# Kernel tuning notes

Measured on AMD Instinct MI355X. Metric: run time of the kernel, lower is better.

The kernel has to match this reference:

```python
import jax, jax.numpy as jnp
import numpy as np

N_ATOMS = 100_000
N_PAIRS = 3_200_000


def setup_inputs() -> dict:
    key = jax.random.key(0)
    k0, k1, k2, k3, k4 = jax.random.split(key, 5)
    atomic_numbers = jax.random.randint(k0, (N_ATOMS,), 1, 95, dtype=jnp.int32)
    distances = jax.random.uniform(k1, (N_PAIRS,), jnp.float32, 0.5, 5.0)
    cutoffs = jax.random.uniform(k2, (N_PAIRS,), jnp.float32)
    idx_i = jnp.sort(jax.random.randint(k3, (N_PAIRS,), 0, N_ATOMS, dtype=jnp.int32))
    idx_j = jax.random.randint(k4, (N_PAIRS,), 0, N_ATOMS, dtype=jnp.int32)
    # ZBL parameters (trainable=True defaults from __init__)
    a_coefficient = jnp.array([0.8854], dtype=jnp.float32)
    a_exponent = jnp.array([0.23], dtype=jnp.float32)
    phi_coefficients = jnp.array([0.18175, 0.50986, 0.28022, 0.02817], dtype=jnp.float32)
    phi_exponents = jnp.array([3.1998, 0.94229, 0.4029, 0.20162], dtype=jnp.float32)
    # unit conversion buffers: identity units -> factors = 1.0
    ke = jnp.array([1.0 / (4.0 * np.pi * 0.005526349406)], dtype=jnp.float32)
    distances_model2Ang = jnp.array([1.0], dtype=jnp.float32)
    energies_Hatree2model = jnp.array([1.0], dtype=jnp.float32)
    return dict(atomic_numbers=atomic_numbers, distances=distances, cutoffs=cutoffs,
                idx_i=idx_i, idx_j=idx_j, a_coefficient=a_coefficient,
                a_exponent=a_exponent, phi_coefficients=phi_coefficients,
                phi_exponents=phi_exponents, ke=ke,
                distances_model2Ang=distances_model2Ang,
                energies_Hatree2model=energies_Hatree2model)


def reference(atomic_numbers, distances, cutoffs, idx_i, idx_j,
              a_coefficient, a_exponent, phi_coefficients, phi_exponents,
              ke, distances_model2Ang, energies_Hatree2model):
    Z = atomic_numbers.astype(distances.dtype)            # [N]
    distances_ang = distances * distances_model2Ang        # [P]
    za = Z ** jnp.abs(a_exponent)                          # [N] (a_exponent is [1])
    a_ij = jnp.abs(a_coefficient) / (za[idx_i] + za[idx_j])  # [P]
    arguments = distances / a_ij                           # [P] (faithful: uses model-unit distances)
    # L1-normalized |phi_coefficients|
    abs_c = jnp.abs(phi_coefficients)
    coefficients = abs_c / jnp.sum(abs_c)                  # [4]
    exponents = jnp.abs(phi_exponents)                     # [4]
    # phi[p] = sum_k c_k * exp(-e_k * arg_p)  -> [P,4] intermediate
    phi = jnp.sum(coefficients[None, :] * jnp.exp(-exponents[None, :] * arguments[:, None]), axis=1)
    repulsion = ke * Z[idx_i] * Z[idx_j] / distances_ang * phi * cutoffs  # [P]
    Erep = energies_Hatree2model * jax.ops.segment_sum(repulsion, idx_i, num_segments=N_ATOMS)
    return Erep
```

## Files before the change

kernel.cpp:

```cpp
#include <hip/hip_runtime.h>
#include <hip/hip_bf16.h>
#include <math.h>

#define LOG2E 1.4426950408889634f

__global__ void __launch_bounds__(256)
zbl_prep(const int* __restrict__ Z, unsigned char* __restrict__ z8,
         float* __restrict__ out, int n_atoms, int out_n) {
    int i = blockIdx.x * blockDim.x + threadIdx.x;
    if (i < n_atoms) z8[i] = (unsigned char)Z[i];
    if (i < out_n)   out[i] = 0.0f;
}

template <typename ZT>
__global__ void __launch_bounds__(256)
zbl_pairs(const float* __restrict__ dist, const float* __restrict__ cut,
          const int* __restrict__ idx_i, const int* __restrict__ idx_j,
          const ZT* __restrict__ zt,
          const float* __restrict__ a_coef, const float* __restrict__ a_exp,
          const float* __restrict__ phi_c, const float* __restrict__ phi_e,
          const float* __restrict__ ke, const float* __restrict__ d2a,
          const float* __restrict__ e2m,
          float* __restrict__ out, int n) {
    __shared__ float za_tab[128];

    float aexp   = fabsf(a_exp[0]);
    float inv_ac = __fdividef(1.0f, fabsf(a_coef[0]));
    float c0 = fabsf(phi_c[0]), c1 = fabsf(phi_c[1]),
          c2 = fabsf(phi_c[2]), c3 = fabsf(phi_c[3]);
    float cnorm = __fdividef(1.0f, c0 + c1 + c2 + c3);
    c0 *= cnorm; c1 *= cnorm; c2 *= cnorm; c3 *= cnorm;
    float e0 = fabsf(phi_e[0]) * LOG2E, e1 = fabsf(phi_e[1]) * LOG2E,
          e2 = fabsf(phi_e[2]) * LOG2E, e3 = fabsf(phi_e[3]) * LOG2E;
    float scale = ke[0] * e2m[0];
    float inv_d2a = __fdividef(1.0f, d2a[0]);

    int t = threadIdx.x;
    if (t < 128) za_tab[t] = powf((float)t, aexp);
    __syncthreads();

    int p = blockIdx.x * blockDim.x + t;

    int   ii  = -1;
    float val = 0.0f;
    if (p < n) {
        ii = idx_i[p];
        int jj = idx_j[p];
        int zi = (int)zt[ii];
        int zj = (int)zt[jj];
        float zif = (float)zi, zjf = (float)zj;
        float d   = dist[p];
        float arg = d * (za_tab[zi] + za_tab[zj]) * inv_ac;
        float phi = c0 * exp2f(-e0 * arg) + c1 * exp2f(-e1 * arg)
                  + c2 * exp2f(-e2 * arg) + c3 * exp2f(-e3 * arg);
        float invd = __fdividef(1.0f, d);
        val = scale * zif * zjf * phi * cut[p] * invd * inv_d2a;
    }

    int lane = t & 63;
    #pragma unroll
    for (int off = 1; off < 64; off <<= 1) {
        float ov = __shfl_up(val, (unsigned)off, 64);
        int   oi = __shfl_up(ii, (unsigned)off, 64);
        if (lane >= off && oi == ii) val += ov;
    }
    int nxt = __shfl_down(ii, 1u, 64);
    bool tail = (lane == 63) || (nxt != ii);
    if (p < n && tail) atomicAdd(out + ii, val);
}

extern "C" void kernel_launch(void* const* d_in, const int* in_sizes, int n_in,
                              void* d_out, int out_size, void* d_ws, size_t ws_size,
                              hipStream_t stream) {
    const int*   atomic_numbers = (const int*)  d_in[0];
    const float* distances      = (const float*)d_in[1];
    const float* cutoffs        = (const float*)d_in[2];
    const int*   idx_i          = (const int*)  d_in[3];
    const int*   idx_j          = (const int*)  d_in[4];
    const float* a_coefficient  = (const float*)d_in[5];
    const float* a_exponent     = (const float*)d_in[6];
    const float* phi_coeffs     = (const float*)d_in[7];
    const float* phi_exps       = (const float*)d_in[8];
    const float* ke             = (const float*)d_in[9];
    const float* d2a            = (const float*)d_in[10];
    const float* e2m            = (const float*)d_in[11];
    float* out = (float*)d_out;

    const int n_atoms = in_sizes[0];
    const int n_pairs = in_sizes[1];

    const int block = 256;
    const int grid_pairs = (n_pairs + block - 1) / block;
    const int grid_prep  = (((n_atoms > out_size) ? n_atoms : out_size) + block - 1) / block;

    if (ws_size >= (size_t)n_atoms) {
        unsigned char* z8 = (unsigned char*)d_ws;
        zbl_prep<<<grid_prep, block, 0, stream>>>(
            atomic_numbers, z8, out, n_atoms, out_size);
        zbl_pairs<unsigned char><<<grid_pairs, block, 0, stream>>>(
            distances, cutoffs, idx_i, idx_j, z8,
            a_coefficient, a_exponent, phi_coeffs, phi_exps, ke, d2a, e2m,
            out, n_pairs);
    } else {
        hipMemsetAsync(d_out, 0, (size_t)out_size * sizeof(float), stream);
        zbl_pairs<int><<<grid_pairs, block, 0, stream>>>(
            distances, cutoffs, idx_i, idx_j, atomic_numbers,
            a_coefficient, a_exponent, phi_coeffs, phi_exps, ke, d2a, e2m,
            out, n_pairs);
    }
}
```

Baseline: 127.4 us.

## Process two pairs per thread with vectorized loads and a segmented scan

New measurement: 122.3 us. 1.04x faster.

```diff
diff --git a/kernel.cpp b/kernel.cpp
--- a/kernel.cpp
+++ b/kernel.cpp
@@ -12,16 +12,15 @@
     if (i < out_n)   out[i] = 0.0f;
 }
 
-template <typename ZT>
 __global__ void __launch_bounds__(256)
-zbl_pairs(const float* __restrict__ dist, const float* __restrict__ cut,
-          const int* __restrict__ idx_i, const int* __restrict__ idx_j,
-          const ZT* __restrict__ zt,
-          const float* __restrict__ a_coef, const float* __restrict__ a_exp,
-          const float* __restrict__ phi_c, const float* __restrict__ phi_e,
-          const float* __restrict__ ke, const float* __restrict__ d2a,
-          const float* __restrict__ e2m,
-          float* __restrict__ out, int n) {
+zbl_pairs2(const float* __restrict__ dist, const float* __restrict__ cut,
+           const int* __restrict__ idx_i, const int* __restrict__ idx_j,
+           const unsigned char* __restrict__ z8,
+           const float* __restrict__ a_coef, const float* __restrict__ a_exp,
+           const float* __restrict__ phi_c, const float* __restrict__ phi_e,
+           const float* __restrict__ ke, const float* __restrict__ d2a,
+           const float* __restrict__ e2m,
+           float* __restrict__ out, int n) {
     __shared__ float za_tab[128];
 
     float aexp   = fabsf(a_exp[0]);
@@ -32,41 +31,67 @@
     c0 *= cnorm; c1 *= cnorm; c2 *= cnorm; c3 *= cnorm;
     float e0 = fabsf(phi_e[0]) * LOG2E, e1 = fabsf(phi_e[1]) * LOG2E,
           e2 = fabsf(phi_e[2]) * LOG2E, e3 = fabsf(phi_e[3]) * LOG2E;
-    float scale = ke[0] * e2m[0];
-    float inv_d2a = __fdividef(1.0f, d2a[0]);
+    float scale = ke[0] * e2m[0] * __fdividef(1.0f, d2a[0]);
 
     int t = threadIdx.x;
-    if (t < 128) za_tab[t] = powf((float)t, aexp);
+    if (t < 128) za_tab[t] = (t >= 1) ? exp2f(aexp * __log2f((float)t)) : 0.0f;
     __syncthreads();
 
-    int p = blockIdx.x * blockDim.x + t;
+    int gid = blockIdx.x * blockDim.x + t;
+    int p0 = 2 * gid, p1 = p0 + 1;
 
-    int   ii  = -1;
-    float val = 0.0f;
-    if (p < n) {
-        ii = idx_i[p];
-        int jj = idx_j[p];
-        int zi = (int)zt[ii];
-        int zj = (int)zt[jj];
-        float zif = (float)zi, zjf = (float)zj;
-        float d   = dist[p];
+    int   k0 = -1, k1 = -1;
+    float v0 = 0.0f, v1 = 0.0f;
+
+    if (p1 < n) {
+        float2 d2 = ((const float2*)dist)[gid];
+        float2 c2v = ((const float2*)cut)[gid];
+        int2   i2 = ((const int2*)idx_i)[gid];
+        int2   j2 = ((const int2*)idx_j)[gid];
+        k0 = i2.x; k1 = i2.y;
+        int zi0 = (int)z8[k0],  zi1 = (int)z8[k1];
+        int zj0 = (int)z8[j2.x], zj1 = (int)z8[j2.y];
+
+        float arg0 = d2.x * (za_tab[zi0] + za_tab[zj0]) * inv_ac;
+        float arg1 = d2.y * (za_tab[zi1] + za_tab[zj1]) * inv_ac;
+        float phi0 = c0 * exp2f(-e0 * arg0) + c1 * exp2f(-e1 * arg0)
+                   + c2 * exp2f(-e2 * arg0) + c3 * exp2f(-e3 * arg0);
+        float phi1 = c0 * exp2f(-e0 * arg1) + c1 * exp2f(-e1 * arg1)
+                   + c2 * exp2f(-e2 * arg1) + c3 * exp2f(-e3 * arg1);
+        v0 = scale * (float)(zi0 * zj0) * phi0 * c2v.x * __fdividef(1.0f, d2.x);
+        v1 = scale * (float)(zi1 * zj1) * phi1 * c2v.y * __fdividef(1.0f, d2.y);
+    } else if (p0 < n) {
+        k0 = idx_i[p0];
+        int jj = idx_j[p0];
+        int zi = (int)z8[k0], zj = (int)z8[jj];
+        float d = dist[p0];
         float arg = d * (za_tab[zi] + za_tab[zj]) * inv_ac;
         float phi = c0 * exp2f(-e0 * arg) + c1 * exp2f(-e1 * arg)
                   + c2 * exp2f(-e2 * arg) + c3 * exp2f(-e3 * arg);
-        float invd = __fdividef(1.0f, d);
-        val = scale * zif * zjf * phi * cut[p] * invd * inv_d2a;
+        v0 = scale * (float)(zi * zj) * phi * cut[p0] * __fdividef(1.0f, d);
     }
+
+    float c = v1 + ((k0 == k1) ? v0 : 0.0f);
+    int   key = k1;
 
     int lane = t & 63;
     #pragma unroll
     for (int off = 1; off < 64; off <<= 1) {
-        float ov = __shfl_up(val, (unsigned)off, 64);
-        int   oi = __shfl_up(ii, (unsigned)off, 64);
-        if (lane >= off && oi == ii) val += ov;
+        float ov = __shfl_up(c, (unsigned)off, 64);
+        int   ok = __shfl_up(key, (unsigned)off, 64);
+        if (lane >= off && ok == key) c += ov;
     }
-    int nxt = __shfl_down(ii, 1u, 64);
-    bool tail = (lane == 63) || (nxt != ii);
-    if (p < n && tail) atomicAdd(out + ii, val);
+
+    float prev_c   = __shfl_up(c, 1u, 64);
+    int   prev_key = __shfl_up(key, 1u, 64);
+    int   next_k0  = __shfl_down(k0, 1u, 64);
+
+    if (k0 >= 0 && k0 != k1) {
+        float tot = v0 + ((lane > 0 && prev_key == k0) ? prev_c : 0.0f);
+        atomicAdd(out + k0, tot);
+    }
+    bool tail = (lane == 63) || (next_k0 != key);
+    if (key >= 0 && tail) atomicAdd(out + key, c);
 }
 
 extern "C" void kernel_launch(void* const* d_in, const int* in_sizes, int n_in,
@@ -90,22 +115,15 @@
     const int n_pairs = in_sizes[1];
 
     const int block = 256;
-    const int grid_pairs = (n_pairs + block - 1) / block;
+    const int n_threads = (n_pairs + 1) / 2;
+    const int grid_pairs = (n_threads + block - 1) / block;
     const int grid_prep  = (((n_atoms > out_size) ? n_atoms : out_size) + block - 1) / block;
 
-    if (ws_size >= (size_t)n_atoms) {
-        unsigned char* z8 = (unsigned char*)d_ws;
-        zbl_prep<<<grid_prep, block, 0, stream>>>(
-            atomic_numbers, z8, out, n_atoms, out_size);
-        zbl_pairs<unsigned char><<<grid_pairs, block, 0, stream>>>(
-            distances, cutoffs, idx_i, idx_j, z8,
-            a_coefficient, a_exponent, phi_coeffs, phi_exps, ke, d2a, e2m,
-            out, n_pairs);
-    } else {
-        hipMemsetAsync(d_out, 0, (size_t)out_size * sizeof(float), stream);
-        zbl_pairs<int><<<grid_pairs, block, 0, stream>>>(
-            distances, cutoffs, idx_i, idx_j, atomic_numbers,
-            a_coefficient, a_exponent, phi_coeffs, phi_exps, ke, d2a, e2m,
-            out, n_pairs);
-    }
+    unsigned char* z8 = (unsigned char*)d_ws;
+    zbl_prep<<<grid_prep, block, 0, stream>>>(
+        atomic_numbers, z8, out, n_atoms, out_size);
+    zbl_pairs2<<<grid_pairs, block, 0, stream>>>(
+        distances, cutoffs, idx_i, idx_j, z8,
+        a_coefficient, a_exponent, phi_coeffs, phi_exps, ke, d2a, e2m,
+        out, n_pairs);
 }
```
